# Optimization experiments

Hardware: AMD Instinct MI355X
Metric: run time of the kernel (lower is better)

## Reference

```python
import jax, jax.numpy as jnp
import numpy as np

B, N, DIM, H = 64, 196, 1024, 32
HD = DIM // H  # 32, must equal H for the bias broadcast quirk
S = 14  # sqrt(num_patches)


def _relative_position_index(s):
    coords = np.stack(np.meshgrid(np.arange(s), np.arange(s), indexing='ij'))  # [2,s,s]
    cf = coords.reshape(2, -1)  # [2, N]
    rel = (cf[:, :, None] - cf[:, None, :]).transpose(1, 2, 0)  # [N,N,2]
    rel[..., 0] += s - 1
    rel[..., 1] += s - 1
    rel[..., 0] *= 2 * s - 1
    return rel.sum(-1).astype(np.int32)  # [N,N], values in [0, (2s-1)^2)


def setup_inputs() -> dict:
    key = jax.random.key(0)
    k0, k1, k2, k3 = jax.random.split(key, 4)
    x = jax.random.normal(k0, (B, N, DIM), dtype=jnp.float32)
    W_qkv = jax.random.normal(k1, (DIM, 3 * DIM), dtype=jnp.float32) * 0.02
    W_proj = jax.random.normal(k2, (DIM, DIM), dtype=jnp.float32) * 0.02
    b_proj = jnp.zeros((DIM,), dtype=jnp.float32)
    rpk = jax.random.normal(k3, ((2 * S - 1) ** 2, HD), dtype=jnp.float32)  # [729, HD]
    rel_idx = jnp.asarray(_relative_position_index(S))  # [N, N] int32
    return {"x": x, "W_qkv": W_qkv, "W_proj": W_proj, "b_proj": b_proj,
            "rpk": rpk, "rel_idx": rel_idx}


def reference(x, W_qkv, W_proj, b_proj, rpk, rel_idx):
    b, n, c = x.shape
    scale = HD ** -0.5
    qkv = (x @ W_qkv).reshape(b, n, 3, H, HD)  # [B,N,3,H,HD]
    q, k, v = jnp.moveaxis(qkv, 2, 0)          # each [B,N,H,HD]
    q = q.transpose(0, 2, 1, 3)                # [B,H,N,HD]
    k = k.transpose(0, 2, 1, 3)
    v = v.transpose(0, 2, 1, 3)
    attn = jnp.einsum('bhnd,bhmd->bhnm', q, k) * scale  # [B,H,N,N]
    # gather relative-position bias: [N*N, HD] -> [N,N,HD] -> [HD,N,N]
    bias = rpk[rel_idx.reshape(-1)].reshape(n, n, HD).transpose(2, 0, 1)
    attn = jax.nn.softmax(attn + bias[None], axis=-1)   # bias broadcasts since HD == H
    out = jnp.einsum('bhnm,bhmd->bhnd', attn, v)        # [B,H,N,HD]
    out = out.transpose(0, 2, 1, 3).reshape(b, n, c)    # [B,N,C]
    return out @ W_proj + b_proj
```

## Files before the change

kernel.cpp:

```cpp
#include <hip/hip_runtime.h>
#include <hip/hip_bf16.h>

typedef __bf16 bf16_t;
typedef __attribute__((ext_vector_type(8))) __bf16 bf16x8;
typedef __attribute__((ext_vector_type(4))) __bf16 bf16x4;
typedef __attribute__((ext_vector_type(4))) float f32x4;

#define NPOS 38416
#define NPAD 224
#define KSTR 40
#define VSTR 232

__device__ __forceinline__ void async_copy16(const bf16_t* g, bf16_t* l) {
  __builtin_amdgcn_global_load_lds((const __attribute__((address_space(1))) void*)g,
                                   (__attribute__((address_space(3))) void*)l, 16, 0, 0);
}

__global__ __launch_bounds__(256) void cast_x_kernel(const float* __restrict__ x,
                                                     bf16_t* __restrict__ xb, int n4) {
  int i = blockIdx.x * 256 + threadIdx.x;
  if (i < n4) {
    float4 v = ((const float4*)x)[i];
    bf16x4 o;
    o[0] = (bf16_t)v.x; o[1] = (bf16_t)v.y; o[2] = (bf16_t)v.z; o[3] = (bf16_t)v.w;
    ((bf16x4*)xb)[i] = o;
  }
}

__global__ __launch_bounds__(256) void transpose_cast_kernel(const float* __restrict__ src,
                                                             bf16_t* __restrict__ dst,
                                                             int K, int Ncols) {
  __shared__ float tile[32][33];
  int t = threadIdx.x;
  int tx = t & 31, ty = t >> 5;
  int bx = blockIdx.x, by = blockIdx.y;
  for (int r = ty; r < 32; r += 8)
    tile[r][tx] = src[(size_t)(by * 32 + r) * Ncols + bx * 32 + tx];
  __syncthreads();
  for (int r = ty; r < 32; r += 8)
    dst[(size_t)(bx * 32 + r) * K + by * 32 + tx] = (bf16_t)tile[tx][r];
}

__global__ __launch_bounds__(256) void bias_gather_kernel(const float* __restrict__ rpk,
                                                          const int* __restrict__ rel_idx,
                                                          float* __restrict__ bias) {
  int pos = blockIdx.x * 256 + threadIdx.x;
  if (pos < NPOS) {
    int idx = rel_idx[pos];
    const float* r = rpk + idx * 32;
#pragma unroll
    for (int h = 0; h < 32; ++h) bias[h * NPOS + pos] = r[h];
  }
}

#define GSTAGE(KT)                                                            \
  do {                                                                        \
    _Pragma("unroll") for (int _j = 0; _j < 4; ++_j)                          \
        async_copy16(gp[_j] + (KT) * 32, &Sh[(KT) & 3][lofs[_j]]);            \
  } while (0)

#define KSTEP(IT, VN)                                                         \
  do {                                                                        \
    __builtin_amdgcn_sched_barrier(0);                                        \
    asm volatile("s_waitcnt vmcnt(" VN ")" ::: "memory");                     \
    __builtin_amdgcn_s_barrier();                                             \
    __builtin_amdgcn_sched_barrier(0);                                        \
    const bf16_t* Sb = &Sh[(IT) & 3][0];                                      \
    bf16x8 af[8], bfr[4];                                                     \
    _Pragma("unroll") for (int _i = 0; _i < 8; ++_i)                          \
        af[_i] = *(const bf16x8*)(Sb + (wrp + _i) * 512 + qoff);              \
    _Pragma("unroll") for (int _j = 0; _j < 4; ++_j)                          \
        bfr[_j] = *(const bf16x8*)(Sb + 8192 + (wcp + _j) * 512 + qoff);      \
    __builtin_amdgcn_s_setprio(1);                                            \
    _Pragma("unroll") for (int _i = 0; _i < 8; ++_i)                          \
        _Pragma("unroll") for (int _j = 0; _j < 4; ++_j)                      \
            acc[_i][_j] = __builtin_amdgcn_mfma_f32_16x16x32_bf16(            \
                af[_i], bfr[_j], acc[_i][_j], 0, 0, 0);                       \
    __builtin_amdgcn_s_setprio(0);                                            \
    __builtin_amdgcn_sched_barrier(0);                                        \
    __builtin_amdgcn_s_barrier();                                             \
  } while (0)

template <int MODE>
__global__ __launch_bounds__(512, 2) void gemm_bt_kernel(
    const bf16_t* __restrict__ A, const bf16_t* __restrict__ Bt,
    bf16_t* __restrict__ qo, bf16_t* __restrict__ ko, bf16_t* __restrict__ vto,
    float* __restrict__ fo, const float* __restrict__ bp) {
  constexpr int K = 1024;
  __shared__ alignas(16) bf16_t Sh[4][16384];
  const int t = threadIdx.x;
  const int lane = t & 63;
  const int quad = lane >> 4;
  const int l16 = lane & 15;
  const int wave = t >> 6;
  const int m0 = blockIdx.y * 256, n0 = blockIdx.x * 256;
  const int wr = (wave >> 2) * 128, wc = (wave & 3) * 64;
  const int wrp = wr >> 4, wcp = wc >> 4;
  const int qoff = quad * 128 + l16 * 8;

  const bf16_t* gp[4];
  int lofs[4];
#pragma unroll
  for (int j = 0; j < 4; ++j) {
    const int p = wave * 4 + j;
    const int pr = (p < 16 ? p : p - 16) * 16 + l16;
    gp[j] = (p < 16) ? A + (size_t)(m0 + pr) * K + quad * 8
                     : Bt + (size_t)(n0 + pr) * K + quad * 8;
    lofs[j] = p * 512 + lane * 8;
  }

  const f32x4 vzero = {0.f, 0.f, 0.f, 0.f};
  f32x4 acc[8][4];
#pragma unroll
  for (int i = 0; i < 8; ++i)
#pragma unroll
    for (int j = 0; j < 4; ++j) acc[i][j] = vzero;

  GSTAGE(0);
  GSTAGE(1);
  GSTAGE(2);

  for (int it = 0; it < 29; ++it) {
    GSTAGE(it + 3);
    KSTEP(it, "12");
  }
  KSTEP(29, "8");
  KSTEP(30, "4");
  KSTEP(31, "0");

  if (MODE == 0) {
    const float qscale = 0.17677669529663687f;
    const int which = n0 >> 10;
#pragma unroll
    for (int i = 0; i < 8; ++i) {
      const int rb = m0 + wr + i * 16 + quad * 4;
#pragma unroll
      for (int j = 0; j < 4; ++j) {
        const int c = n0 + wc + j * 16 + l16;
        const int h = (c >> 5) & 31, d = c & 31;
#pragma unroll
        for (int r = 0; r < 4; ++r) {
          const int rg = rb + r;
          const int b = rg / 196, n = rg - b * 196;
          const float v = acc[i][j][r];
          if (which == 0)
            qo[(((size_t)b * 32 + h) * 196 + n) * 32 + d] = (bf16_t)(v * qscale);
          else if (which == 1)
            ko[(((size_t)b * 32 + h) * 196 + n) * 32 + d] = (bf16_t)v;
          else
            vto[(((size_t)b * 32 + h) * 32 + d) * 196 + n] = (bf16_t)v;
        }
      }
    }
  } else {
#pragma unroll
    for (int i = 0; i < 8; ++i) {
      const int rb = m0 + wr + i * 16 + quad * 4;
#pragma unroll
      for (int j = 0; j < 4; ++j) {
        const int c = n0 + wc + j * 16 + l16;
        const float bias_c = bp[c];
#pragma unroll
        for (int r = 0; r < 4; ++r)
          fo[(size_t)(rb + r) * 1024 + c] = acc[i][j][r] + bias_c;
      }
    }
  }
}

__global__ __launch_bounds__(256, 2) void attn_kernel(
    const bf16_t* __restrict__ q, const bf16_t* __restrict__ kmat,
    const bf16_t* __restrict__ vtg, const float* __restrict__ bias,
    bf16_t* __restrict__ attn_out) {
  __shared__ alignas(16) bf16_t kf[NPAD * KSTR];
  __shared__ alignas(16) bf16_t vts[32 * VSTR];
  __shared__ alignas(16) bf16_t pb[4][16 * VSTR];

  const int t = threadIdx.x;
  const int lane = t & 63;
  const int quad = lane >> 4, l16 = lane & 15;
  const int wave = t >> 6;
  const int bh = blockIdx.x;
  const int b = bh >> 5, h = bh & 31;
  const bf16_t* qg = q + (size_t)bh * (196 * 32);
  const bf16_t* kg = kmat + (size_t)bh * (196 * 32);
  const bf16_t* vg = vtg + (size_t)bh * (32 * 196);
  const float* bg = bias + (size_t)h * NPOS;

  {
    const uint4* src = (const uint4*)kg;
    uint4* dst = (uint4*)kf;
    for (int c = t; c < 784; c += 256) dst[(c >> 2) * 5 + (c & 3)] = src[c];
    const uint4 z4 = {0u, 0u, 0u, 0u};
    if (t < 112) {
      int r = 196 + (t >> 2), ch = t & 3;
      dst[r * 5 + ch] = z4;
    }
    const uint2 z2 = {0u, 0u};
    for (int i = t; i < 1792; i += 256) {
      int d = i / 56, c = i - d * 56;
      uint2 val = (c < 49) ? ((const uint2*)(vg + d * 196))[c] : z2;
      ((uint2*)(vts + d * VSTR))[c] = val;
    }
  }
  __syncthreads();

  const f32x4 vzero = {0.f, 0.f, 0.f, 0.f};
  bf16_t* pw = &pb[wave][0];

  for (int ch = wave; ch < 13; ch += 4) {
    const int q0 = ch * 16;
    int qrow = q0 + l16;
    if (qrow > 195) qrow = 195;
    const bf16x8 aq = *(const bf16x8*)(qg + qrow * 32 + quad * 8);

    float bv[13][4];
#pragma unroll
    for (int ct = 0; ct < 13; ++ct) {
      const int col = ct * 16 + l16;
#pragma unroll
      for (int r = 0; r < 4; ++r) {
        int br = q0 + quad * 4 + r;
        if (br > 195) br = 195;
        bv[ct][r] = (col < 196) ? bg[br * 196 + col] : 0.f;
      }
    }

    f32x4 s[13];
#pragma unroll
    for (int ct = 0; ct < 13; ++ct) {
      const bf16x8 bk = *(const bf16x8*)(kf + (ct * 16 + l16) * KSTR + quad * 8);
      s[ct] = __builtin_amdgcn_mfma_f32_16x16x32_bf16(aq, bk, vzero, 0, 0, 0);
    }
#pragma unroll
    for (int ct = 0; ct < 13; ++ct) {
      const int col = ct * 16 + l16;
#pragma unroll
      for (int r = 0; r < 4; ++r) {
        if (col < 196)
          s[ct][r] += bv[ct][r];
        else
          s[ct][r] = -1e30f;
      }
    }
    float mx[4], inv[4];
#pragma unroll
    for (int r = 0; r < 4; ++r) {
      float m = s[0][r];
#pragma unroll
      for (int ct = 1; ct < 13; ++ct) m = fmaxf(m, s[ct][r]);
      m = fmaxf(m, __shfl_xor(m, 1));
      m = fmaxf(m, __shfl_xor(m, 2));
      m = fmaxf(m, __shfl_xor(m, 4));
      m = fmaxf(m, __shfl_xor(m, 8));
      mx[r] = m;
    }
#pragma unroll
    for (int ct = 0; ct < 13; ++ct)
#pragma unroll
      for (int r = 0; r < 4; ++r) s[ct][r] = __expf(s[ct][r] - mx[r]);
#pragma unroll
    for (int r = 0; r < 4; ++r) {
      float sum = s[0][r];
#pragma unroll
      for (int ct = 1; ct < 13; ++ct) sum += s[ct][r];
      sum += __shfl_xor(sum, 1);
      sum += __shfl_xor(sum, 2);
      sum += __shfl_xor(sum, 4);
      sum += __shfl_xor(sum, 8);
      inv[r] = 1.f / sum;
    }
#pragma unroll
    for (int ct = 0; ct < 13; ++ct) {
      const int col = ct * 16 + l16;
#pragma unroll
      for (int r = 0; r < 4; ++r) pw[(quad * 4 + r) * VSTR + col] = (bf16_t)s[ct][r];
    }
    if (lane < 32) {
      const bf16x8 z8 = {};
      *(bf16x8*)(pw + (lane >> 1) * VSTR + 208 + (lane & 1) * 8) = z8;
    }
#pragma unroll
    for (int dt = 0; dt < 2; ++dt) {
      f32x4 o = vzero;
#pragma unroll
      for (int kk = 0; kk < 7; ++kk) {
        const bf16x8 ap = *(const bf16x8*)(pw + l16 * VSTR + kk * 32 + quad * 8);
        const bf16x8 bv2 = *(const bf16x8*)(vts + (dt * 16 + l16) * VSTR + kk * 32 + quad * 8);
        o = __builtin_amdgcn_mfma_f32_16x16x32_bf16(ap, bv2, o, 0, 0, 0);
      }
      const int d = dt * 16 + l16;
#pragma unroll
      for (int r = 0; r < 4; ++r) {
        const int n = q0 + quad * 4 + r;
        if (n < 196)
          attn_out[(((size_t)b * 196 + n) * 32 + h) * 32 + d] = (bf16_t)(o[r] * inv[r]);
      }
    }
  }
}

extern "C" void kernel_launch(void* const* d_in, const int* in_sizes, int n_in,
                              void* d_out, int out_size, void* d_ws, size_t ws_size,
                              hipStream_t stream) {
  (void)in_sizes; (void)n_in; (void)out_size; (void)ws_size;
  const float* x = (const float*)d_in[0];
  const float* Wqkv = (const float*)d_in[1];
  const float* Wproj = (const float*)d_in[2];
  const float* bproj = (const float*)d_in[3];
  const float* rpk = (const float*)d_in[4];
  const int* rel_idx = (const int*)d_in[5];
  float* out = (float*)d_out;

  char* ws = (char*)d_ws;
  bf16_t* xb = (bf16_t*)(ws + 0);
  bf16_t* wqkvT = (bf16_t*)(ws + 25690112);
  bf16_t* wprojT = (bf16_t*)(ws + 31981568);
  bf16_t* q = (bf16_t*)(ws + 34078720);
  bf16_t* kk = (bf16_t*)(ws + 59768832);
  bf16_t* vt = (bf16_t*)(ws + 85458944);
  float* bias = (float*)(ws + 111149056);
  bf16_t* attn = xb;

  cast_x_kernel<<<12544, 256, 0, stream>>>(x, xb, 12845056 / 4);
  transpose_cast_kernel<<<dim3(96, 32), 256, 0, stream>>>(Wqkv, wqkvT, 1024, 3072);
  transpose_cast_kernel<<<dim3(32, 32), 256, 0, stream>>>(Wproj, wprojT, 1024, 1024);
  bias_gather_kernel<<<151, 256, 0, stream>>>(rpk, rel_idx, bias);
  gemm_bt_kernel<0><<<dim3(12, 49), 512, 0, stream>>>(xb, wqkvT, q, kk, vt, nullptr, nullptr);
  attn_kernel<<<2048, 256, 0, stream>>>(q, kk, vt, bias, attn);
  gemm_bt_kernel<1><<<dim3(4, 49), 512, 0, stream>>>(attn, wprojT, nullptr, nullptr, nullptr, out, bproj);
}
```

Measured before the change: 377.2 us.

## Split GEMM k-step into two ping-pong phases and swizzle workgroups across XCDs

```diff
diff --git a/kernel.cpp b/kernel.cpp
--- a/kernel.cpp
+++ b/kernel.cpp
@@ -53,33 +53,50 @@
   }
 }
 
-#define GSTAGE(KT)                                                            \
-  do {                                                                        \
-    _Pragma("unroll") for (int _j = 0; _j < 4; ++_j)                          \
-        async_copy16(gp[_j] + (KT) * 32, &Sh[(KT) & 3][lofs[_j]]);            \
-  } while (0)
-
-#define KSTEP(IT, VN)                                                         \
-  do {                                                                        \
-    __builtin_amdgcn_sched_barrier(0);                                        \
-    asm volatile("s_waitcnt vmcnt(" VN ")" ::: "memory");                     \
-    __builtin_amdgcn_s_barrier();                                             \
-    __builtin_amdgcn_sched_barrier(0);                                        \
-    const bf16_t* Sb = &Sh[(IT) & 3][0];                                      \
-    bf16x8 af[8], bfr[4];                                                     \
-    _Pragma("unroll") for (int _i = 0; _i < 8; ++_i)                          \
-        af[_i] = *(const bf16x8*)(Sb + (wrp + _i) * 512 + qoff);              \
-    _Pragma("unroll") for (int _j = 0; _j < 4; ++_j)                          \
-        bfr[_j] = *(const bf16x8*)(Sb + 8192 + (wcp + _j) * 512 + qoff);      \
-    __builtin_amdgcn_s_setprio(1);                                            \
-    _Pragma("unroll") for (int _i = 0; _i < 8; ++_i)                          \
-        _Pragma("unroll") for (int _j = 0; _j < 4; ++_j)                      \
-            acc[_i][_j] = __builtin_amdgcn_mfma_f32_16x16x32_bf16(            \
-                af[_i], bfr[_j], acc[_i][_j], 0, 0, 0);                       \
-    __builtin_amdgcn_s_setprio(0);                                            \
-    __builtin_amdgcn_sched_barrier(0);                                        \
-    __builtin_amdgcn_s_barrier();                                             \
-  } while (0)
+#define PHASE_A(NU, DOSTAGE)                                                   \
+  {                                                                            \
+    const bf16_t* Sb = &Sh[(NU) & 3][0];                                       \
+    _Pragma("unroll") for (int _i = 0; _i < 4; ++_i)                           \
+        afA[_i] = *(const bf16x8*)(Sb + (wrp + _i) * 512 + qoff);              \
+    _Pragma("unroll") for (int _j = 0; _j < 4; ++_j)                           \
+        bfr[_j] = *(const bf16x8*)(Sb + 8192 + (wcp + _j) * 512 + qoff);       \
+    if (DOSTAGE) {                                                             \
+      async_copy16(gp[0] + ((NU) + 2) * 32, &Sh[((NU) + 2) & 3][lofs[0]]);     \
+      async_copy16(gp[1] + ((NU) + 2) * 32, &Sh[((NU) + 2) & 3][lofs[1]]);     \
+    }                                                                          \
+    __builtin_amdgcn_s_barrier();                                              \
+    asm volatile("s_waitcnt lgkmcnt(0)" ::: "memory");                         \
+    __builtin_amdgcn_sched_barrier(0);                                         \
+    __builtin_amdgcn_s_setprio(1);                                             \
+    _Pragma("unroll") for (int _i = 0; _i < 4; ++_i)                           \
+        _Pragma("unroll") for (int _j = 0; _j < 4; ++_j)                       \
+            acc[_i][_j] = __builtin_amdgcn_mfma_f32_16x16x32_bf16(             \
+                afA[_i], bfr[_j], acc[_i][_j], 0, 0, 0);                       \
+    __builtin_amdgcn_s_setprio(0);                                             \
+    __builtin_amdgcn_s_barrier();                                              \
+  }
+
+#define PHASE_B(NU, DOSTAGE, VMS)                                              \
+  {                                                                            \
+    const bf16_t* Sb = &Sh[(NU) & 3][0];                                       \
+    _Pragma("unroll") for (int _i = 0; _i < 4; ++_i)                           \
+        afB[_i] = *(const bf16x8*)(Sb + (wrp + 4 + _i) * 512 + qoff);          \
+    if (DOSTAGE) {                                                             \
+      async_copy16(gp[2] + ((NU) + 2) * 32, &Sh[((NU) + 2) & 3][lofs[2]]);     \
+      async_copy16(gp[3] + ((NU) + 2) * 32, &Sh[((NU) + 2) & 3][lofs[3]]);     \
+    }                                                                          \
+    __builtin_amdgcn_s_barrier();                                              \
+    asm volatile("s_waitcnt lgkmcnt(0)" ::: "memory");                         \
+    __builtin_amdgcn_sched_barrier(0);                                         \
+    __builtin_amdgcn_s_setprio(1);                                             \
+    _Pragma("unroll") for (int _i = 0; _i < 4; ++_i)                           \
+        _Pragma("unroll") for (int _j = 0; _j < 4; ++_j)                       \
+            acc[4 + _i][_j] = __builtin_amdgcn_mfma_f32_16x16x32_bf16(         \
+                afB[_i], bfr[_j], acc[4 + _i][_j], 0, 0, 0);                   \
+    __builtin_amdgcn_s_setprio(0);                                             \
+    asm volatile("s_waitcnt vmcnt(" VMS ")" ::: "memory");                     \
+    __builtin_amdgcn_s_barrier();                                              \
+  }
 
 template <int MODE>
 __global__ __launch_bounds__(512, 2) void gemm_bt_kernel(
@@ -93,7 +110,15 @@
   const int quad = lane >> 4;
   const int l16 = lane & 15;
   const int wave = t >> 6;
-  const int m0 = blockIdx.y * 256, n0 = blockIdx.x * 256;
+
+  const int GX = gridDim.x;
+  const int nwg = GX * gridDim.y;
+  const int lin = blockIdx.y * GX + blockIdx.x;
+  const int qch = nwg >> 3, rch = nwg & 7;
+  const int xcd = lin & 7, off = lin >> 3;
+  const int swz = (xcd < rch ? xcd * (qch + 1) : rch * (qch + 1) + (xcd - rch) * qch) + off;
+  const int m0 = (swz / GX) * 256, n0 = (swz % GX) * 256;
+
   const int wr = (wave >> 2) * 128, wc = (wave & 3) * 64;
   const int wrp = wr >> 4, wcp = wc >> 4;
   const int qoff = quad * 128 + l16 * 8;
@@ -116,17 +141,23 @@
 #pragma unroll
     for (int j = 0; j < 4; ++j) acc[i][j] = vzero;
 
-  GSTAGE(0);
-  GSTAGE(1);
-  GSTAGE(2);
-
-  for (int it = 0; it < 29; ++it) {
-    GSTAGE(it + 3);
-    KSTEP(it, "12");
-  }
-  KSTEP(29, "8");
-  KSTEP(30, "4");
-  KSTEP(31, "0");
+  bf16x8 afA[4], afB[4], bfr[4];
+
+#pragma unroll
+  for (int j = 0; j < 4; ++j) async_copy16(gp[j], &Sh[0][lofs[j]]);
+#pragma unroll
+  for (int j = 0; j < 4; ++j) async_copy16(gp[j] + 32, &Sh[1][lofs[j]]);
+  asm volatile("s_waitcnt vmcnt(4)" ::: "memory");
+  __builtin_amdgcn_s_barrier();
+
+  for (int n = 0; n < 30; ++n) {
+    PHASE_A(n, true);
+    PHASE_B(n, true, "4");
+  }
+  PHASE_A(30, false);
+  PHASE_B(30, false, "0");
+  PHASE_A(31, false);
+  PHASE_B(31, false, "0");
 
   if (MODE == 0) {
     const float qscale = 0.17677669529663687f;
```

Result: faster. 368.5 us (-2.3%).
